# Performance work log

Measured on AMD Instinct MI355X. Metric: run time of the kernel, lower is better.

## Reference

```python
import jax, jax.numpy as jnp
import numpy as np

B, T, N, D = 64, 12, 207, 128
H, ORDER = 8, 2
HID = 2 * D  # mlp_ratio = 2


def _ln(x, g, b, eps=1e-5):
    m = x.mean(-1, keepdims=True)
    v = ((x - m) ** 2).mean(-1, keepdims=True)
    return (x - m) * jax.lax.rsqrt(v + eps) * g + b


def _l2norm(t, eps=1e-12):
    # matches torch.nn.functional.normalize(dim=-1)
    n = jnp.sqrt((t * t).sum(-1, keepdims=True))
    return t / jnp.maximum(n, eps)


def _fast_attn(q, k, v):
    # q, k, v: (B2, L, H, Dh); Performer-style linear attention from FastAttentionLayer.fast_attention
    q = _l2norm(q)
    k = _l2norm(k)
    L = q.shape[1]
    kvs = jnp.einsum('blhm,blhd->bhmd', k, v)
    num = jnp.einsum('bnhm,bhmd->bnhd', q, kvs) + L * v
    ks_sum = k.sum(axis=1)  # (B2, H, Dh)
    den = jnp.einsum('bnhm,bhm->bnh', q, ks_sum)[..., None] + L
    return num / jnp.maximum(den, 1e-5)


def _fast_layer(x, qkv_w, out_w, out_b):
    # x: (B, T, N, D). qkv_bias=False (mask arg), kernel=3 -> out_proj: Linear(2D, D)
    b, t, n, d = x.shape
    dh = d // H
    qkv = x @ qkv_w.T  # (B, T, N, 3D)
    q, k, v = jnp.split(qkv, 3, axis=-1)
    # spatial pass: attend over the N nodes for each (b, t)
    out_s = _fast_attn(q.reshape(b * t, n, H, dh),
                       k.reshape(b * t, n, H, dh),
                       v.reshape(b * t, n, H, dh)).reshape(b, t, n, d)
    # temporal pass: attend over the T steps for each (b, n)
    qt = q.transpose(0, 2, 1, 3).reshape(b * n, t, H, dh)
    kt = k.transpose(0, 2, 1, 3).reshape(b * n, t, H, dh)
    vt = v.transpose(0, 2, 1, 3).reshape(b * n, t, H, dh)
    out_t = _fast_attn(qt, kt, vt).reshape(b, n, t, d).transpose(0, 2, 1, 3)
    return jnp.concatenate([out_s, out_t], -1) @ out_w.T + out_b


def _forward(x, graph, qkv_w, out_w, out_b, pw_w, pw_b,
             fc1_w, fc1_b, fc2_w, fc2_b, ln1_g, ln1_b, ln2_g, ln2_b):
    # GraphPropagate: x_list = [x, graph @ x, ...] (Ks = ORDER hops)
    xs = [x]
    xk = x
    for _ in range(ORDER - 1):
        xk = jnp.einsum('thi,btij->bthj', graph, xk)
        xs.append(xk)
    # per-hop fast attention + zero-init pointwise branch, summed over hops
    agg = jnp.zeros_like(x)
    for i in range(ORDER):
        agg = agg + _fast_layer(xs[i], qkv_w[i], out_w[i], out_b[i]) + xs[i] @ pw_w[i].T + pw_b[i]
    h = _ln(x + agg, ln1_g, ln1_b)
    ff = jax.nn.relu(h @ fc1_w.T + fc1_b) @ fc2_w.T + fc2_b
    return _ln(h + ff, ln2_g, ln2_b)


def setup_inputs() -> dict:
    key = jax.random.key(0)
    ks = jax.random.split(key, 8)
    s = 0.02
    return {
        'x': jax.random.normal(ks[0], (B, T, N, D), jnp.float32),
        'graph': jax.random.uniform(ks[1], (T, N, N), jnp.float32) / N,
        'qkv_w': jax.random.normal(ks[2], (ORDER, 3 * D, D), jnp.float32) * s,
        'out_w': jax.random.normal(ks[3], (ORDER, D, 2 * D), jnp.float32) * s,
        'out_b': jnp.zeros((ORDER, D), jnp.float32),
        'pw_w': jax.random.normal(ks[4], (ORDER, D, D), jnp.float32) * s,
        'pw_b': jnp.zeros((ORDER, D), jnp.float32),
        'fc1_w': jax.random.normal(ks[5], (HID, D), jnp.float32) * s,
        'fc1_b': jnp.zeros((HID,), jnp.float32),
        'fc2_w': jax.random.normal(ks[6], (D, HID), jnp.float32) * s,
        'fc2_b': jnp.zeros((D,), jnp.float32),
        'ln1_g': jnp.ones((D,), jnp.float32),
        'ln1_b': jnp.zeros((D,), jnp.float32),
        'ln2_g': jnp.ones((D,), jnp.float32),
        'ln2_b': jnp.zeros((D,), jnp.float32),
    }


def reference(x, graph, qkv_w, out_w, out_b, pw_w, pw_b,
              fc1_w, fc1_b, fc2_w, fc2_b, ln1_g, ln1_b, ln2_g, ln2_b):
    return _forward(x, graph, qkv_w, out_w, out_b, pw_w, pw_b,
                    fc1_w, fc1_b, fc2_w, fc2_b, ln1_g, ln1_b, ln2_g, ln2_b)
```

## Files before the change

### kernel.cpp

```cpp
#include <hip/hip_runtime.h>
#include <hip/hip_bf16.h>

#define BB 64
#define TT 12
#define NN 207
#define DD 128
#define HH 8
#define DH 16
#define MROWS (BB*TT*NN)
#define KPAD 224
#define AW 768
#define CHB 32
#define CROWS (CHB*TT*NN)

typedef __bf16 bf16x8 __attribute__((ext_vector_type(8)));
typedef __bf16 bf16x4 __attribute__((ext_vector_type(4)));
typedef float  f32x4  __attribute__((ext_vector_type(4)));

__device__ inline float  b2f(__bf16 v){ return (float)v; }
__device__ inline __bf16 f2b(float v){ return (__bf16)v; }
__device__ inline bf16x8 ldfrag(const __bf16* p){ return *reinterpret_cast<const bf16x8*>(p); }

__device__ inline void gload_lds16(const __bf16* g, __bf16* l){
    __builtin_amdgcn_global_load_lds(
        (const __attribute__((address_space(1))) void*)(g),
        (__attribute__((address_space(3))) void*)(l), 16, 0, 0);
}
__device__ inline int swz(int r){ return (r ^ (r>>2)) & 3; }

__global__ __launch_bounds__(256) void xcopy_kernel(const float* __restrict__ x, __bf16* __restrict__ abuf)
{
    int nt = gridDim.x*256;
    for (int gIdx = blockIdx.x*256 + threadIdx.x; gIdx < MROWS*16; gIdx += nt) {
        int row = gIdx >> 4, c8 = (gIdx & 15)*8;
        const float* s = x + (size_t)row*DD + c8;
        f32x4 a = *reinterpret_cast<const f32x4*>(s);
        f32x4 b = *reinterpret_cast<const f32x4*>(s+4);
        bf16x8 r;
        #pragma unroll
        for (int i=0;i<4;i++){ r[i] = f2b(a[i]); r[i+4] = f2b(b[i]); }
        *reinterpret_cast<bf16x8*>(abuf + (size_t)row*AW + c8) = r;
    }
}

__global__ __launch_bounds__(256) void prep_misc_kernel(
    const float* __restrict__ graph, const float* __restrict__ qkv_w,
    const float* __restrict__ out_w, const float* __restrict__ out_b,
    const float* __restrict__ pw_w,  const float* __restrict__ pw_b,
    const float* __restrict__ fc1_w, const float* __restrict__ fc2_w,
    __bf16* __restrict__ gpad, __bf16* __restrict__ qkv_wb, __bf16* __restrict__ wcomb,
    __bf16* __restrict__ fc1_wb, __bf16* __restrict__ fc2_wb, float* __restrict__ bias_comb)
{
    int nt = gridDim.x*256;
    int tid = blockIdx.x*256 + threadIdx.x;
    for (int i = tid; i < TT*NN*KPAD; i += nt) {
        int k = i % KPAD, r = i / KPAD;
        gpad[i] = (k < NN) ? f2b(graph[(size_t)r*NN + k]) : f2b(0.f);
    }
    for (int i = tid; i < 2*3*DD*DD; i += nt) qkv_wb[i] = f2b(qkv_w[i]);
    for (int i = tid; i < DD*AW; i += nt) {
        int c = i / AW, j = i % AW;
        float v;
        if      (j < 128) v = pw_w[c*128 + j];
        else if (j < 256) v = pw_w[128*128 + c*128 + (j-128)];
        else if (j < 512) v = out_w[c*256 + (j-256)];
        else              v = out_w[128*256 + c*256 + (j-512)];
        wcomb[i] = f2b(v);
    }
    for (int i = tid; i < 2*DD*DD; i += nt) fc1_wb[i] = f2b(fc1_w[i]);
    for (int i = tid; i < 2*DD*DD; i += nt) fc2_wb[i] = f2b(fc2_w[i]);
    for (int i = tid; i < DD; i += nt)
        bias_comb[i] = pw_b[i] + pw_b[128+i] + out_b[i] + out_b[128+i];
}

__global__ __launch_bounds__(256) void propagate_kernel(const __bf16* __restrict__ gp,
    __bf16* __restrict__ abuf)
{
    int bt   = blockIdx.x;
    int t    = bt % TT;
    int tile = blockIdx.y;
    int lane = threadIdx.x & 63, w = threadIdx.x >> 6;
    int lhi = lane >> 4, llo = lane & 15;
    __shared__ __attribute__((aligned(16))) __bf16 XT[DD][40];
    const __bf16* xbt  = abuf + (size_t)bt*NN*AW;
    const __bf16* grow = gp + (size_t)t*NN*KPAD;
    int rowbase = tile*64 + w*16;
    f32x4 acc[8];
    #pragma unroll
    for (int i=0;i<8;i++) acc[i] = (f32x4){0.f,0.f,0.f,0.f};
    int arow = rowbase + llo; if (arow > NN-1) arow = NN-1;
    for (int k0=0; k0<KPAD; k0+=32) {
        __syncthreads();
        for (int kl = (threadIdx.x>>7); kl < 32; kl += 2) {
            int kk = k0 + kl, c = threadIdx.x & 127;
            XT[c][kl] = (kk < NN) ? xbt[(size_t)kk*AW + c] : f2b(0.f);
        }
        __syncthreads();
        bf16x8 a = ldfrag(grow + (size_t)arow*KPAD + k0 + lhi*8);
        #pragma unroll
        for (int cf=0;cf<8;cf++){
            bf16x8 b = *reinterpret_cast<const bf16x8*>(&XT[cf*16+llo][lhi*8]);
            acc[cf] = __builtin_amdgcn_mfma_f32_16x16x32_bf16(a, b, acc[cf], 0,0,0);
        }
    }
    #pragma unroll
    for (int e=0;e<4;e++){
        int row = rowbase + lhi*4 + e;
        if (row < NN) {
            #pragma unroll
            for (int cf=0;cf<8;cf++)
                abuf[((size_t)bt*NN + row)*AW + DD + cf*16 + llo] = f2b(acc[cf][e]);
        }
    }
}

template<int MODE, bool RELU>
__global__ __launch_bounds__(512) void gemm_kernel(const __bf16* __restrict__ A, size_t lda,
    const __bf16* __restrict__ W, const float* __restrict__ bias,
    void* out, size_t ldc, int K, int mend,
    const __bf16* __restrict__ resid, size_t ldr,
    const float* __restrict__ lng, const float* __restrict__ lnb)
{
    __shared__ __attribute__((aligned(16))) __bf16 lds[3][12288];
    int w = threadIdx.x >> 6, lane = threadIdx.x & 63;
    int lhi = lane >> 4, llo = lane & 15;
    size_t row0 = (size_t)blockIdx.x*256;
    int col0 = blockIdx.y*128;
    int nt = K >> 5;

    int sA0 = (w*2+0)*64 + lane, sA1 = (w*2+1)*64 + lane, sW = w*64 + lane;
    int rA0 = sA0>>2, uA0 = sA0&3, rA1 = sA1>>2, uA1 = sA1&3, rW = sW>>2, uW = sW&3;
    long gr0 = (long)row0 + rA0; if (gr0 >= mend) gr0 = mend-1;
    long gr1 = (long)row0 + rA1; if (gr1 >= mend) gr1 = mend-1;
    const __bf16* gA0 = A + (size_t)gr0*lda + ((uA0 ^ swz(rA0))<<3);
    const __bf16* gA1 = A + (size_t)gr1*lda + ((uA1 ^ swz(rA1))<<3);
    const __bf16* gW  = W + (size_t)(col0 + rW)*K + ((uW ^ swz(rW))<<3);
    __bf16* base0 = &lds[0][0];

    int aoff[2], woff[8];
    #pragma unroll
    for (int rt=0;rt<2;rt++){
        int rl = w*32 + rt*16 + llo;
        aoff[rt] = rl*32 + ((lhi ^ swz(rl))<<3);
    }
    #pragma unroll
    for (int cf=0;cf<8;cf++){
        int wr = cf*16 + llo;
        woff[cf] = 8192 + wr*32 + ((lhi ^ swz(wr))<<3);
    }

    f32x4 acc[2][8];
    #pragma unroll
    for (int i=0;i<2;i++)
        #pragma unroll
        for (int j=0;j<8;j++) acc[i][j] = (f32x4){0.f,0.f,0.f,0.f};

    #define STAGE(buf, tt) { int k0 = (tt)<<5; __bf16* Lw = base0 + (buf)*12288;           \
        gload_lds16(gA0 + k0, Lw + (w*2+0)*512);                                           \
        gload_lds16(gA1 + k0, Lw + (w*2+1)*512);                                           \
        gload_lds16(gW  + k0, Lw + 8192 + w*512); }

    STAGE(0,0); STAGE(1,1); STAGE(2,2);

    int cur = 0;
    for (int t = 0; t < nt; ++t) {
        if (t <= nt-3)      asm volatile("s_waitcnt vmcnt(6)" ::: "memory");
        else if (t == nt-2) asm volatile("s_waitcnt vmcnt(3)" ::: "memory");
        else                asm volatile("s_waitcnt vmcnt(0)" ::: "memory");
        __builtin_amdgcn_s_barrier();
        __builtin_amdgcn_sched_barrier(0);
        const __bf16* Lb = base0 + cur*12288;
        bf16x8 a[2], b[8];
        #pragma unroll
        for (int rt=0;rt<2;rt++) a[rt] = *reinterpret_cast<const bf16x8*>(&Lb[aoff[rt]]);
        #pragma unroll
        for (int cf=0;cf<8;cf++)  b[cf] = *reinterpret_cast<const bf16x8*>(&Lb[woff[cf]]);
        asm volatile("s_waitcnt lgkmcnt(0)" ::: "memory");
        __builtin_amdgcn_sched_barrier(0);
        __builtin_amdgcn_s_barrier();
        if (t+3 < nt) STAGE(cur, t+3);
        #pragma unroll
        for (int rt=0;rt<2;rt++)
            #pragma unroll
            for (int cf=0;cf<8;cf++)
                acc[rt][cf] = __builtin_amdgcn_mfma_f32_16x16x32_bf16(a[rt], b[cf], acc[rt][cf], 0,0,0);
        cur = (cur == 2) ? 0 : cur + 1;
    }
    #undef STAGE

    float bv[8];
    #pragma unroll
    for (int cf=0;cf<8;cf++) bv[cf] = bias ? bias[col0 + cf*16 + llo] : 0.f;

    if (MODE == 0) {
        #pragma unroll
        for (int rt=0;rt<2;rt++) {
            #pragma unroll
            for (int e=0;e<4;e++) {
                size_t row = row0 + (size_t)w*32 + rt*16 + lhi*4 + e;
                if ((long)row >= mend) continue;
                #pragma unroll
                for (int cf=0;cf<8;cf++) {
                    float v = acc[rt][cf][e] + bv[cf];
                    if (RELU) v = fmaxf(v, 0.f);
                    ((__bf16*)out)[row*ldc + col0 + cf*16 + llo] = f2b(v);
                }
            }
        }
    } else {
        float g8[8], b8[8];
        #pragma unroll
        for (int cf=0;cf<8;cf++){ int c = cf*16 + llo; g8[cf] = lng[c]; b8[cf] = lnb[c]; }
        #pragma unroll
        for (int rt=0;rt<2;rt++) {
            #pragma unroll
            for (int e=0;e<4;e++) {
                size_t row = row0 + (size_t)w*32 + rt*16 + lhi*4 + e;
                if ((long)row >= mend) continue;
                float vals[8], s = 0.f, ss = 0.f;
                #pragma unroll
                for (int cf=0;cf<8;cf++) {
                    int c = cf*16 + llo;
                    float r = b2f(resid[row*ldr + c]);
                    float v = acc[rt][cf][e] + bv[cf] + r;
                    vals[cf] = v; s += v; ss += v*v;
                }
                #pragma unroll
                for (int o=1;o<16;o<<=1){ s += __shfl_xor(s,o,64); ss += __shfl_xor(ss,o,64); }
                float mean = s * (1.f/DD);
                float var  = ss * (1.f/DD) - mean*mean;
                float rs   = rsqrtf(var + 1e-5f);
                #pragma unroll
                for (int cf=0;cf<8;cf++) {
                    float v = (vals[cf]-mean)*rs*g8[cf] + b8[cf];
                    size_t idx = row*ldc + cf*16 + llo;
                    if (MODE == 3) ((__bf16*)out)[idx] = f2b(v);
                    else           ((float*)out)[idx]  = v;
                }
            }
        }
    }
}

template<bool RELU>
__global__ __launch_bounds__(256) void sgemm_k128(const __bf16* __restrict__ A, size_t lda,
    const __bf16* __restrict__ W, const float* __restrict__ bias,
    __bf16* __restrict__ out, size_t ldc, int ngroups)
{
    __shared__ __attribute__((aligned(16))) __bf16 lds[12][2048];
    int w = threadIdx.x >> 6, lane = threadIdx.x & 63;
    int lhi = lane >> 4, llo = lane & 15;
    int col0 = blockIdx.y*128;

    bf16x8 wf[4][8];
    #pragma unroll
    for (int ks=0;ks<4;ks++)
        #pragma unroll
        for (int cf=0;cf<8;cf++)
            wf[ks][cf] = ldfrag(W + (size_t)(col0 + cf*16 + llo)*128 + ks*32 + lhi*8);

    f32x4 bvv[8];
    #pragma unroll
    for (int cf=0;cf<8;cf++){
        if (bias) bvv[cf] = *reinterpret_cast<const f32x4*>(bias + col0 + cf*16 + lhi*4);
        else      bvv[cf] = (f32x4){0.f,0.f,0.f,0.f};
    }

    size_t gsrc[4];
    #pragma unroll
    for (int j=0;j<4;j++){
        int r = j*4 + lhi;
        int u = llo ^ r;
        gsrc[j] = (size_t)r*lda + (size_t)u*8;
    }
    int aoff[4];
    #pragma unroll
    for (int ks=0;ks<4;ks++) aoff[ks] = llo*128 + (((ks<<2)|lhi) ^ llo)*8;

    int gw = blockIdx.x*4 + w, stride = gridDim.x*4;
    int n = (gw < ngroups) ? ((ngroups-1-gw)/stride + 1) : 0;
    __bf16* slab0 = &lds[w*3][0];

    #define SSTAGE(i) { size_t rbase = (size_t)(gw + (size_t)(i)*stride)*16*lda;           \
        __bf16* L = slab0 + ((i)%3)*2048;                                                  \
        gload_lds16(A + rbase + gsrc[0], L);                                               \
        gload_lds16(A + rbase + gsrc[1], L + 512);                                         \
        gload_lds16(A + rbase + gsrc[2], L + 1024);                                        \
        gload_lds16(A + rbase + gsrc[3], L + 1536); }

    if (n > 0) SSTAGE(0);
    if (n > 1) SSTAGE(1);

    for (int i = 0; i < n; ++i) {
        int kept = ((i+1 < n) ? 4 : 0) + ((i >= 2) ? 16 : i*8);
        if      (kept >= 20) asm volatile("s_waitcnt vmcnt(20)" ::: "memory");
        else if (kept == 16) asm volatile("s_waitcnt vmcnt(16)" ::: "memory");
        else if (kept == 12) asm volatile("s_waitcnt vmcnt(12)" ::: "memory");
        else if (kept == 8)  asm volatile("s_waitcnt vmcnt(8)"  ::: "memory");
        else if (kept == 4)  asm volatile("s_waitcnt vmcnt(4)"  ::: "memory");
        else                 asm volatile("s_waitcnt vmcnt(0)"  ::: "memory");

        const __bf16* Ls = slab0 + (i%3)*2048;
        bf16x8 a[4];
        #pragma unroll
        for (int ks=0;ks<4;ks++) a[ks] = *reinterpret_cast<const bf16x8*>(&Ls[aoff[ks]]);

        if (i+2 < n) SSTAGE(i+2);

        f32x4 acc[8];
        #pragma unroll
        for (int cf=0;cf<8;cf++) acc[cf] = (f32x4){0.f,0.f,0.f,0.f};
        #pragma unroll
        for (int ks=0;ks<4;ks++)
            #pragma unroll
            for (int cf=0;cf<8;cf++)
                acc[cf] = __builtin_amdgcn_mfma_f32_16x16x32_bf16(wf[ks][cf], a[ks], acc[cf], 0,0,0);

        size_t grow = (size_t)(gw + (size_t)i*stride)*16 + llo;
        #pragma unroll
        for (int cf=0;cf<8;cf++){
            bf16x4 o;
            #pragma unroll
            for (int e=0;e<4;e++){
                float v = acc[cf][e] + bvv[cf][e];
                if (RELU) v = fmaxf(v, 0.f);
                o[e] = f2b(v);
            }
            *reinterpret_cast<bf16x4*>(out + grow*ldc + col0 + cf*16 + lhi*4) = o;
        }
    }
    #undef SSTAGE
}

#define ACH 32
__global__ __launch_bounds__(256) void attn_s_kernel(const __bf16* __restrict__ qkv,
                                                     __bf16* __restrict__ outp)
{
    int bt = blockIdx.x, g = blockIdx.y;
    const __bf16* base = qkv + (size_t)bt*NN*384 + g*32;
    __shared__ __attribute__((aligned(16))) __bf16 qbuf[224][40];
    __shared__ __attribute__((aligned(16))) __bf16 vbuf[224][40];
    __shared__ __attribute__((aligned(16))) __bf16 kbuf[ACH][40];
    __shared__ float flk[4][16][17];
    __shared__ float fls[4][16];
    int tid = threadIdx.x;
    int wave = tid >> 6, lane = tid & 63;
    int h2 = tid >> 7;
    int dd = tid & 15;
    int oct = ((tid >> 4) & 3) | ((wave & 1) << 2);
    float kvs_col[16]; float ks = 0.f;
    #pragma unroll
    for (int m=0;m<16;m++) kvs_col[m] = 0.f;

    for (int c0 = 0; c0 < NN; c0 += ACH) {
        __syncthreads();
        for (int i = tid; i < ACH*12; i += 256) {
            int r = i/12, u = i%12, seg = u>>2, uu = u&3;
            int nn = c0 + r;
            bf16x8 v8 = (bf16x8){};
            if (nn < NN) v8 = *reinterpret_cast<const bf16x8*>(base + (size_t)nn*384 + seg*128 + uu*8);
            if      (seg == 0) *reinterpret_cast<bf16x8*>(&qbuf[nn][uu*8]) = v8;
            else if (seg == 1) *reinterpret_cast<bf16x8*>(&kbuf[r][uu*8])  = v8;
            else               *reinterpret_cast<bf16x8*>(&vbuf[nn][uu*8]) = v8;
        }
        __syncthreads();
        #pragma unroll
        for (int j=0;j<4;j++){
            int r = oct + 8*j; int nn = c0 + r;
            if (nn >= NN) continue;
            bf16x8 k0 = *reinterpret_cast<const bf16x8*>(&kbuf[r][h2*16]);
            bf16x8 k1 = *reinterpret_cast<const bf16x8*>(&kbuf[r][h2*16+8]);
            float sk = 0.f;
            #pragma unroll
            for (int m=0;m<8;m++){
                float a0=b2f(k0[m]), a1=b2f(k1[m]); sk += a0*a0 + a1*a1;
            }
            float iv = 1.f/fmaxf(sqrtf(sk), 1e-12f);
            float vv  = b2f(vbuf[nn][h2*16+dd]);
            float kdd = b2f(kbuf[r][h2*16+dd]);
            float t2 = iv*vv;
            #pragma unroll
            for (int m=0;m<8;m++){
                kvs_col[m]   += b2f(k0[m])*t2;
                kvs_col[m+8] += b2f(k1[m])*t2;
            }
            ks += kdd*iv;
        }
    }
    #pragma unroll
    for (int m=0;m<16;m++){
        kvs_col[m] += __shfl_xor(kvs_col[m], 16, 64);
        kvs_col[m] += __shfl_xor(kvs_col[m], 32, 64);
    }
    ks += __shfl_xor(ks, 16, 64);
    ks += __shfl_xor(ks, 32, 64);
    if (lane < 16){
        #pragma unroll
        for (int m=0;m<16;m++) flk[wave][m][lane] = kvs_col[m];
        fls[wave][lane] = ks;
    }
    __syncthreads();
    float ksr[16];
    #pragma unroll
    for (int m=0;m<16;m++){
        kvs_col[m] += flk[wave^1][m][dd];
        ksr[m] = fls[h2*2][m] + fls[h2*2+1][m];
    }

    for (int nn = oct; nn < NN; nn += 8) {
        bf16x8 q0 = *reinterpret_cast<const bf16x8*>(&qbuf[nn][h2*16]);
        bf16x8 q1 = *reinterpret_cast<const bf16x8*>(&qbuf[nn][h2*16+8]);
        float sq = 0.f, num = 0.f, den = 0.f;
        #pragma unroll
        for (int m=0;m<8;m++){
            float qm0 = b2f(q0[m]), qm1 = b2f(q1[m]);
            sq  += qm0*qm0 + qm1*qm1;
            num += qm0*kvs_col[m] + qm1*kvs_col[m+8];
            den += qm0*ksr[m]     + qm1*ksr[m+8];
        }
        float iq = 1.f/fmaxf(sqrtf(sq), 1e-12f);
        float vv = b2f(vbuf[nn][h2*16+dd]);
        float o = (num*iq + (float)NN*vv) / fmaxf(den*iq + (float)NN, 1e-5f);
        outp[((size_t)bt*NN + nn)*AW + g*32 + h2*16 + dd] = f2b(o);
    }
}

__global__ __launch_bounds__(256) void attn_t_kernel(const __bf16* __restrict__ qkv,
                                                     __bf16* __restrict__ outp)
{
    int b = blockIdx.x;
    int nn0 = blockIdx.y * 2;
    __shared__ __attribute__((aligned(16))) __bf16 rows[TT][2][384];
    __shared__ float invq[2][TT][8], invk2[2][TT][8];
    int tid = threadIdx.x;
    for (int i = tid; i < TT*2*48; i += 256) {
        int t = i / 96, rem = i % 96;
        int nl = rem / 48, g = rem % 48;
        int nn = nn0 + nl;
        bf16x8 v8 = (bf16x8){};
        if (nn < NN) v8 = *reinterpret_cast<const bf16x8*>(qkv + ((size_t)(b*TT+t)*NN + nn)*384 + g*8);
        *reinterpret_cast<bf16x8*>(&rows[t][nl][g*8]) = v8;
    }
    __syncthreads();
    if (tid < 192) {
        int hh = tid & 7, t = (tid >> 3) % TT, nl = tid / 96;
        bf16x8 q0 = *reinterpret_cast<const bf16x8*>(&rows[t][nl][hh*16]);
        bf16x8 q1 = *reinterpret_cast<const bf16x8*>(&rows[t][nl][hh*16+8]);
        bf16x8 k0 = *reinterpret_cast<const bf16x8*>(&rows[t][nl][128+hh*16]);
        bf16x8 k1 = *reinterpret_cast<const bf16x8*>(&rows[t][nl][128+hh*16+8]);
        float sq = 0.f, sk = 0.f;
        #pragma unroll
        for (int m=0;m<8;m++){
            float a0=b2f(q0[m]), a1=b2f(q1[m]); sq += a0*a0 + a1*a1;
            float c0v=b2f(k0[m]), c1=b2f(k1[m]); sk += c0v*c0v + c1*c1;
        }
        invq[nl][t][hh]  = 1.f/fmaxf(sqrtf(sq), 1e-12f);
        invk2[nl][t][hh] = 1.f/fmaxf(sqrtf(sk), 1e-12f);
    }
    __syncthreads();
    int dd = tid & 15, h = (tid >> 4) & 7, nl = tid >> 7;
    int nn = nn0 + nl;
    float kvs_col[16], ksum[16];
    #pragma unroll
    for (int m=0;m<16;m++){ kvs_col[m]=0.f; ksum[m]=0.f; }
    #pragma unroll
    for (int t=0;t<TT;t++){
        float iv = invk2[nl][t][h];
        bf16x8 k0 = *reinterpret_cast<const bf16x8*>(&rows[t][nl][128+h*16]);
        bf16x8 k1 = *reinterpret_cast<const bf16x8*>(&rows[t][nl][128+h*16+8]);
        float vv = b2f(rows[t][nl][256+h*16+dd]);
        float t2 = iv*vv;
        #pragma unroll
        for (int m=0;m<8;m++){
            float km0 = b2f(k0[m]), km1 = b2f(k1[m]);
            kvs_col[m]   += km0*t2;  ksum[m]   += km0*iv;
            kvs_col[m+8] += km1*t2;  ksum[m+8] += km1*iv;
        }
    }
    #pragma unroll
    for (int t=0;t<TT;t++){
        float iq = invq[nl][t][h];
        bf16x8 q0 = *reinterpret_cast<const bf16x8*>(&rows[t][nl][h*16]);
        bf16x8 q1 = *reinterpret_cast<const bf16x8*>(&rows[t][nl][h*16+8]);
        float num = 0.f, den = 0.f;
        #pragma unroll
        for (int m=0;m<8;m++){
            float qm0 = b2f(q0[m]), qm1 = b2f(q1[m]);
            num += qm0*kvs_col[m]  + qm1*kvs_col[m+8];
            den += qm0*ksum[m]     + qm1*ksum[m+8];
        }
        float vv = b2f(rows[t][nl][256+h*16+dd]);
        float o = (num*iq + (float)TT*vv) / fmaxf(den*iq + (float)TT, 1e-5f);
        if (nn < NN)
            outp[((size_t)(b*TT+t)*NN + nn)*AW + h*16 + dd] = f2b(o);
    }
}

extern "C" void kernel_launch(void* const* d_in, const int* in_sizes, int n_in,
                              void* d_out, int out_size, void* d_ws, size_t ws_size,
                              hipStream_t stream)
{
    const float* x     = (const float*)d_in[0];
    const float* graph = (const float*)d_in[1];
    const float* qkv_w = (const float*)d_in[2];
    const float* out_w = (const float*)d_in[3];
    const float* out_b = (const float*)d_in[4];
    const float* pw_w  = (const float*)d_in[5];
    const float* pw_b  = (const float*)d_in[6];
    const float* fc1_w = (const float*)d_in[7];
    const float* fc1_b = (const float*)d_in[8];
    const float* fc2_w = (const float*)d_in[9];
    const float* fc2_b = (const float*)d_in[10];
    const float* ln1g  = (const float*)d_in[11];
    const float* ln1b  = (const float*)d_in[12];
    const float* ln2g  = (const float*)d_in[13];
    const float* ln2b  = (const float*)d_in[14];
    (void)in_sizes; (void)n_in; (void)out_size; (void)ws_size;

    char* ws = (char*)d_ws;
    size_t off = 0;
    __bf16* abuf = (__bf16*)(ws + off); off += (size_t)MROWS*AW*2;
    __bf16* qkvc = (__bf16*)(ws + off); off += (size_t)CROWS*3*DD*2;
    __bf16* gpad = (__bf16*)(ws + off); off += (size_t)TT*NN*KPAD*2;
    __bf16* qkv_wb = (__bf16*)(ws + off); off += (size_t)2*3*DD*DD*2;
    __bf16* wcomb  = (__bf16*)(ws + off); off += (size_t)DD*AW*2;
    __bf16* fc1_wb = (__bf16*)(ws + off); off += (size_t)2*DD*DD*2;
    __bf16* fc2_wb = (__bf16*)(ws + off); off += (size_t)2*DD*DD*2;
    float*  bias_comb = (float*)(ws + off); off += DD*4;

    dim3 blk(256), blk512(512);

    xcopy_kernel<<<dim3(4096), blk, 0, stream>>>(x, abuf);
    prep_misc_kernel<<<dim3(1024), blk, 0, stream>>>(graph, qkv_w, out_w, out_b, pw_w, pw_b,
        fc1_w, fc2_w, gpad, qkv_wb, wcomb, fc1_wb, fc2_wb, bias_comb);
    propagate_kernel<<<dim3(BB*TT, 4), blk, 0, stream>>>(gpad, abuf);

    for (int hop = 0; hop < 2; ++hop) {
        for (int c = 0; c < BB/CHB; ++c) {
            size_t rowoff = (size_t)c*CROWS;
            sgemm_k128<false><<<dim3(170, 3), blk, 0, stream>>>(
                abuf + rowoff*AW + hop*DD, (size_t)AW, qkv_wb + (size_t)hop*3*DD*DD, nullptr,
                qkvc, (size_t)(3*DD), CROWS/16);
            attn_s_kernel<<<dim3(CHB*TT, 4), blk, 0, stream>>>(
                qkvc, abuf + rowoff*AW + 256 + hop*256);
            attn_t_kernel<<<dim3(CHB, (NN+1)/2), blk, 0, stream>>>(
                qkvc, abuf + rowoff*AW + 384 + hop*256);
        }
    }

    gemm_kernel<3,false><<<dim3(MROWS/256, 1), blk512, 0, stream>>>(
        abuf, (size_t)AW, wcomb, bias_comb, (void*)abuf, (size_t)AW, AW, MROWS,
        abuf, (size_t)AW, ln1g, ln1b);
    sgemm_k128<true><<<dim3(256, 2), blk, 0, stream>>>(
        abuf, (size_t)AW, fc1_wb, fc1_b, abuf + 256, (size_t)AW, MROWS/16);
    gemm_kernel<4,false><<<dim3(MROWS/256, 1), blk512, 0, stream>>>(
        abuf + 256, (size_t)AW, fc2_wb, fc2_b, d_out, (size_t)DD, 2*DD, MROWS,
        abuf, (size_t)AW, ln2g, ln2b);
}
```

Before: 840.8 us.

## Fuse FFN into one kernel, merge attention launches, fold x cast into propagate

Adds an ffn_kernel that computes fc1+ReLU, fc2, the residual and LayerNorm per 128-row tile. The hidden activation stays in LDS instead of going through global memory, and two launches are dropped. The separate spatial and temporal attention kernels are merged into one launch with a block-index split. The standalone fp32-to-bf16 copy of x is removed: propagate now reads fp32 x and writes the bf16 copy itself. Weights in the fused FFN are read directly from global/cache per wave, which may add load pressure.

```diff
diff --git a/kernel.cpp b/kernel.cpp
--- a/kernel.cpp
+++ b/kernel.cpp
@@ -27,21 +27,6 @@
         (__attribute__((address_space(3))) void*)(l), 16, 0, 0);
 }
 __device__ inline int swz(int r){ return (r ^ (r>>2)) & 3; }
-
-__global__ __launch_bounds__(256) void xcopy_kernel(const float* __restrict__ x, __bf16* __restrict__ abuf)
-{
-    int nt = gridDim.x*256;
-    for (int gIdx = blockIdx.x*256 + threadIdx.x; gIdx < MROWS*16; gIdx += nt) {
-        int row = gIdx >> 4, c8 = (gIdx & 15)*8;
-        const float* s = x + (size_t)row*DD + c8;
-        f32x4 a = *reinterpret_cast<const f32x4*>(s);
-        f32x4 b = *reinterpret_cast<const f32x4*>(s+4);
-        bf16x8 r;
-        #pragma unroll
-        for (int i=0;i<4;i++){ r[i] = f2b(a[i]); r[i+4] = f2b(b[i]); }
-        *reinterpret_cast<bf16x8*>(abuf + (size_t)row*AW + c8) = r;
-    }
-}
 
 __global__ __launch_bounds__(256) void prep_misc_kernel(
     const float* __restrict__ graph, const float* __restrict__ qkv_w,
@@ -74,7 +59,7 @@
 }
 
 __global__ __launch_bounds__(256) void propagate_kernel(const __bf16* __restrict__ gp,
-    __bf16* __restrict__ abuf)
+    const float* __restrict__ x, __bf16* __restrict__ abuf)
 {
     int bt   = blockIdx.x;
     int t    = bt % TT;
@@ -82,7 +67,7 @@
     int lane = threadIdx.x & 63, w = threadIdx.x >> 6;
     int lhi = lane >> 4, llo = lane & 15;
     __shared__ __attribute__((aligned(16))) __bf16 XT[DD][40];
-    const __bf16* xbt  = abuf + (size_t)bt*NN*AW;
+    const float*  xbt  = x  + (size_t)bt*NN*DD;
     const __bf16* grow = gp + (size_t)t*NN*KPAD;
     int rowbase = tile*64 + w*16;
     f32x4 acc[8];
@@ -93,7 +78,10 @@
         __syncthreads();
         for (int kl = (threadIdx.x>>7); kl < 32; kl += 2) {
             int kk = k0 + kl, c = threadIdx.x & 127;
-            XT[c][kl] = (kk < NN) ? xbt[(size_t)kk*AW + c] : f2b(0.f);
+            __bf16 xb = (kk < NN) ? f2b(xbt[(size_t)kk*DD + c]) : f2b(0.f);
+            XT[c][kl] = xb;
+            if (kk < NN && (kk>>6) == tile)
+                abuf[((size_t)bt*NN + kk)*AW + c] = xb;
         }
         __syncthreads();
         bf16x8 a = ldfrag(grow + (size_t)arow*KPAD + k0 + lhi*8);
@@ -233,9 +221,7 @@
                 #pragma unroll
                 for (int cf=0;cf<8;cf++) {
                     float v = (vals[cf]-mean)*rs*g8[cf] + b8[cf];
-                    size_t idx = row*ldc + cf*16 + llo;
-                    if (MODE == 3) ((__bf16*)out)[idx] = f2b(v);
-                    else           ((float*)out)[idx]  = v;
+                    ((__bf16*)out)[row*ldc + cf*16 + llo] = f2b(v);
                 }
             }
         }
@@ -332,167 +318,320 @@
     #undef SSTAGE
 }
 
+__global__ __launch_bounds__(256) void ffn_kernel(const __bf16* __restrict__ h,
+    const __bf16* __restrict__ w1, const float* __restrict__ b1,
+    const __bf16* __restrict__ w2, const float* __restrict__ b2,
+    const float* __restrict__ lng, const float* __restrict__ lnb,
+    float* __restrict__ dout)
+{
+    __shared__ __attribute__((aligned(16))) __bf16 hring[3][4096];
+    __shared__ __attribute__((aligned(16))) __bf16 f1b[8192];
+    __shared__ float fl2[32][4][2];
+    int w = threadIdx.x >> 6, lane = threadIdx.x & 63;
+    int lhi = lane >> 4, llo = lane & 15;
+    size_t row0 = (size_t)blockIdx.x * 128;
+
+    size_t gsrc[2]; int ldst[2];
+    #pragma unroll
+    for (int j=0;j<2;j++){
+        int i = w*64 + lane + 256*j;
+        int r = i >> 4, u = i & 15;
+        gsrc[j] = (size_t)r*AW + ((u ^ (r & 15)) << 3);
+        ldst[j] = (w*64 + 256*j) * 8;
+    }
+    #define FSTAGE(slot, g) { const __bf16* src = h + (row0 + (size_t)(g)*32)*AW;          \
+        gload_lds16(src + gsrc[0], &hring[slot][0] + ldst[0]);                             \
+        gload_lds16(src + gsrc[1], &hring[slot][0] + ldst[1]); }
+
+    f32x4 b1v[4], b2v[2], gv[2], bt2[2];
+    #pragma unroll
+    for (int c4=0;c4<4;c4++) b1v[c4] = *reinterpret_cast<const f32x4*>(b1 + w*64 + c4*16 + lhi*4);
+    #pragma unroll
+    for (int c2=0;c2<2;c2++){
+        b2v[c2] = *reinterpret_cast<const f32x4*>(b2  + w*32 + c2*16 + lhi*4);
+        gv[c2]  = *reinterpret_cast<const f32x4*>(lng + w*32 + c2*16 + lhi*4);
+        bt2[c2] = *reinterpret_cast<const f32x4*>(lnb + w*32 + c2*16 + lhi*4);
+    }
+
+    FSTAGE(0,0); FSTAGE(1,1); FSTAGE(2,2);
+
+    for (int g = 0; g < 4; ++g) {
+        if (g < 2)       asm volatile("s_waitcnt vmcnt(4)" ::: "memory");
+        else if (g == 2) asm volatile("s_waitcnt vmcnt(2)" ::: "memory");
+        else             asm volatile("s_waitcnt vmcnt(0)" ::: "memory");
+        __builtin_amdgcn_s_barrier();
+        __builtin_amdgcn_sched_barrier(0);
+        const __bf16* Hs = &hring[g % 3][0];
+
+        bf16x8 hb[2][4];
+        bf16x4 hres[2][2];
+        #pragma unroll
+        for (int rf=0;rf<2;rf++){
+            int r = rf*16 + llo;
+            #pragma unroll
+            for (int ks=0;ks<4;ks++)
+                hb[rf][ks] = *reinterpret_cast<const bf16x8*>(Hs + r*128 + (((ks*4+lhi) ^ llo) << 3));
+            #pragma unroll
+            for (int cf=0;cf<2;cf++){
+                int unit = w*4 + cf*2 + (lhi>>1);
+                hres[cf][rf] = *reinterpret_cast<const bf16x4*>(Hs + r*128 + ((unit ^ llo) << 3) + (lhi & 1)*4);
+            }
+        }
+        asm volatile("s_waitcnt lgkmcnt(0)" ::: "memory");
+        __builtin_amdgcn_sched_barrier(0);
+        __builtin_amdgcn_s_barrier();
+        if (g + 3 < 4) FSTAGE(g % 3, g + 3);
+
+        f32x4 acc1[4][2];
+        #pragma unroll
+        for (int i=0;i<4;i++){ acc1[i][0] = (f32x4){0,0,0,0}; acc1[i][1] = (f32x4){0,0,0,0}; }
+        #pragma unroll
+        for (int ks=0;ks<4;ks++){
+            #pragma unroll
+            for (int cf2=0;cf2<4;cf2++){
+                bf16x8 wfr = ldfrag(w1 + (size_t)(w*64 + cf2*16 + llo)*128 + ks*32 + lhi*8);
+                #pragma unroll
+                for (int rf=0;rf<2;rf++)
+                    acc1[cf2][rf] = __builtin_amdgcn_mfma_f32_16x16x32_bf16(wfr, hb[rf][ks], acc1[cf2][rf], 0,0,0);
+            }
+        }
+        #pragma unroll
+        for (int rf=0;rf<2;rf++){
+            int r = rf*16 + llo;
+            #pragma unroll
+            for (int cf2=0;cf2<4;cf2++){
+                bf16x4 o;
+                #pragma unroll
+                for (int e=0;e<4;e++) o[e] = f2b(fmaxf(acc1[cf2][rf][e] + b1v[cf2][e], 0.f));
+                int unit = w*8 + cf2*2 + (lhi>>1);
+                *reinterpret_cast<bf16x4*>(&f1b[r*256 + ((unit ^ r) << 3) + (lhi&1)*4]) = o;
+            }
+        }
+        asm volatile("s_waitcnt lgkmcnt(0)" ::: "memory");
+        __builtin_amdgcn_sched_barrier(0);
+        __builtin_amdgcn_s_barrier();
+
+        f32x4 acc2[2][2];
+        acc2[0][0]=(f32x4){0,0,0,0}; acc2[0][1]=(f32x4){0,0,0,0};
+        acc2[1][0]=(f32x4){0,0,0,0}; acc2[1][1]=(f32x4){0,0,0,0};
+        #pragma unroll
+        for (int ks2=0;ks2<8;ks2++){
+            bf16x8 fb[2];
+            #pragma unroll
+            for (int rf=0;rf<2;rf++){
+                int r = rf*16 + llo;
+                fb[rf] = *reinterpret_cast<const bf16x8*>(&f1b[r*256 + (((ks2*4+lhi) ^ r) << 3)]);
+            }
+            #pragma unroll
+            for (int cf=0;cf<2;cf++){
+                bf16x8 wfr = ldfrag(w2 + (size_t)(w*32 + cf*16 + llo)*256 + ks2*32 + lhi*8);
+                #pragma unroll
+                for (int rf=0;rf<2;rf++)
+                    acc2[cf][rf] = __builtin_amdgcn_mfma_f32_16x16x32_bf16(wfr, fb[rf], acc2[cf][rf], 0,0,0);
+            }
+        }
+
+        float vals[2][2][4]; float s[2] = {0.f,0.f}, ss[2] = {0.f,0.f};
+        #pragma unroll
+        for (int rf=0;rf<2;rf++)
+            #pragma unroll
+            for (int cf=0;cf<2;cf++)
+                #pragma unroll
+                for (int e=0;e<4;e++){
+                    float v = acc2[cf][rf][e] + b2v[cf][e] + b2f(hres[cf][rf][e]);
+                    vals[rf][cf][e] = v; s[rf] += v; ss[rf] += v*v;
+                }
+        #pragma unroll
+        for (int rf=0;rf<2;rf++){
+            s[rf]  += __shfl_xor(s[rf],16,64);  s[rf]  += __shfl_xor(s[rf],32,64);
+            ss[rf] += __shfl_xor(ss[rf],16,64); ss[rf] += __shfl_xor(ss[rf],32,64);
+            if (lhi == 0){ fl2[rf*16+llo][w][0] = s[rf]; fl2[rf*16+llo][w][1] = ss[rf]; }
+        }
+        asm volatile("s_waitcnt lgkmcnt(0)" ::: "memory");
+        __builtin_amdgcn_s_barrier();
+        #pragma unroll
+        for (int rf=0;rf<2;rf++){
+            int r = rf*16 + llo;
+            float S  = fl2[r][0][0]+fl2[r][1][0]+fl2[r][2][0]+fl2[r][3][0];
+            float SS = fl2[r][0][1]+fl2[r][1][1]+fl2[r][2][1]+fl2[r][3][1];
+            float mean = S*(1.f/DD), var = SS*(1.f/DD)-mean*mean, rs = rsqrtf(var+1e-5f);
+            size_t grow = row0 + (size_t)g*32 + r;
+            #pragma unroll
+            for (int cf=0;cf<2;cf++){
+                f32x4 o;
+                #pragma unroll
+                for (int e=0;e<4;e++) o[e] = (vals[rf][cf][e]-mean)*rs*gv[cf][e] + bt2[cf][e];
+                *reinterpret_cast<f32x4*>(dout + grow*DD + w*32 + cf*16 + lhi*4) = o;
+            }
+        }
+        __builtin_amdgcn_s_barrier();
+    }
+    #undef FSTAGE
+}
+
 #define ACH 32
-__global__ __launch_bounds__(256) void attn_s_kernel(const __bf16* __restrict__ qkv,
-                                                     __bf16* __restrict__ outp)
+#define SBLKS (CHB*TT*4)
+__global__ __launch_bounds__(256) void attn_st_kernel(const __bf16* __restrict__ qkv,
+    __bf16* __restrict__ outs, __bf16* __restrict__ outt)
 {
-    int bt = blockIdx.x, g = blockIdx.y;
-    const __bf16* base = qkv + (size_t)bt*NN*384 + g*32;
-    __shared__ __attribute__((aligned(16))) __bf16 qbuf[224][40];
-    __shared__ __attribute__((aligned(16))) __bf16 vbuf[224][40];
-    __shared__ __attribute__((aligned(16))) __bf16 kbuf[ACH][40];
-    __shared__ float flk[4][16][17];
-    __shared__ float fls[4][16];
+    __shared__ __attribute__((aligned(16))) char smem[44032];
     int tid = threadIdx.x;
-    int wave = tid >> 6, lane = tid & 63;
-    int h2 = tid >> 7;
-    int dd = tid & 15;
-    int oct = ((tid >> 4) & 3) | ((wave & 1) << 2);
-    float kvs_col[16]; float ks = 0.f;
-    #pragma unroll
-    for (int m=0;m<16;m++) kvs_col[m] = 0.f;
-
-    for (int c0 = 0; c0 < NN; c0 += ACH) {
+    int bx = blockIdx.x;
+
+    if (bx < SBLKS) {
+        int bt = bx >> 2, g = bx & 3;
+        const __bf16* base = qkv + (size_t)bt*NN*384 + g*32;
+        __bf16 (*qbuf)[40] = (__bf16(*)[40])(smem);
+        __bf16 (*vbuf)[40] = (__bf16(*)[40])(smem + 17920);
+        __bf16 (*kbuf)[40] = (__bf16(*)[40])(smem + 35840);
+        float (*flk)[16][17] = (float(*)[16][17])(smem + 38400);
+        float (*fls)[16]     = (float(*)[16])(smem + 42752);
+        int wave = tid >> 6, lane = tid & 63;
+        int h2 = tid >> 7;
+        int dd = tid & 15;
+        int oct = ((tid >> 4) & 3) | ((wave & 1) << 2);
+        float kvs_col[16]; float ks = 0.f;
+        #pragma unroll
+        for (int m=0;m<16;m++) kvs_col[m] = 0.f;
+
+        for (int c0 = 0; c0 < NN; c0 += ACH) {
+            __syncthreads();
+            for (int i = tid; i < ACH*12; i += 256) {
+                int r = i/12, u = i%12, seg = u>>2, uu = u&3;
+                int nn = c0 + r;
+                bf16x8 v8 = (bf16x8){};
+                if (nn < NN) v8 = *reinterpret_cast<const bf16x8*>(base + (size_t)nn*384 + seg*128 + uu*8);
+                if      (seg == 0) *reinterpret_cast<bf16x8*>(&qbuf[nn][uu*8]) = v8;
+                else if (seg == 1) *reinterpret_cast<bf16x8*>(&kbuf[r][uu*8])  = v8;
+                else               *reinterpret_cast<bf16x8*>(&vbuf[nn][uu*8]) = v8;
+            }
+            __syncthreads();
+            #pragma unroll
+            for (int j=0;j<4;j++){
+                int r = oct + 8*j; int nn = c0 + r;
+                if (nn >= NN) continue;
+                bf16x8 k0 = *reinterpret_cast<const bf16x8*>(&kbuf[r][h2*16]);
+                bf16x8 k1 = *reinterpret_cast<const bf16x8*>(&kbuf[r][h2*16+8]);
+                float sk = 0.f;
+                #pragma unroll
+                for (int m=0;m<8;m++){
+                    float a0=b2f(k0[m]), a1=b2f(k1[m]); sk += a0*a0 + a1*a1;
+                }
+                float iv = 1.f/fmaxf(sqrtf(sk), 1e-12f);
+                float vv  = b2f(vbuf[nn][h2*16+dd]);
+                float kdd = b2f(kbuf[r][h2*16+dd]);
+                float t2 = iv*vv;
+                #pragma unroll
+                for (int m=0;m<8;m++){
+                    kvs_col[m]   += b2f(k0[m])*t2;
+                    kvs_col[m+8] += b2f(k1[m])*t2;
+                }
+                ks += kdd*iv;
+            }
+        }
+        #pragma unroll
+        for (int m=0;m<16;m++){
+            kvs_col[m] += __shfl_xor(kvs_col[m], 16, 64);
+            kvs_col[m] += __shfl_xor(kvs_col[m], 32, 64);
+        }
+        ks += __shfl_xor(ks, 16, 64);
+        ks += __shfl_xor(ks, 32, 64);
+        if (lane < 16){
+            #pragma unroll
+            for (int m=0;m<16;m++) flk[wave][m][lane] = kvs_col[m];
+            fls[wave][lane] = ks;
+        }
         __syncthreads();
-        for (int i = tid; i < ACH*12; i += 256) {
-            int r = i/12, u = i%12, seg = u>>2, uu = u&3;
-            int nn = c0 + r;
+        float ksr[16];
+        #pragma unroll
+        for (int m=0;m<16;m++){
+            kvs_col[m] += flk[wave^1][m][dd];
+            ksr[m] = fls[h2*2][m] + fls[h2*2+1][m];
+        }
+        for (int nn = oct; nn < NN; nn += 8) {
+            bf16x8 q0 = *reinterpret_cast<const bf16x8*>(&qbuf[nn][h2*16]);
+            bf16x8 q1 = *reinterpret_cast<const bf16x8*>(&qbuf[nn][h2*16+8]);
+            float sq = 0.f, num = 0.f, den = 0.f;
+            #pragma unroll
+            for (int m=0;m<8;m++){
+                float qm0 = b2f(q0[m]), qm1 = b2f(q1[m]);
+                sq  += qm0*qm0 + qm1*qm1;
+                num += qm0*kvs_col[m] + qm1*kvs_col[m+8];
+                den += qm0*ksr[m]     + qm1*ksr[m+8];
+            }
+            float iq = 1.f/fmaxf(sqrtf(sq), 1e-12f);
+            float vv = b2f(vbuf[nn][h2*16+dd]);
+            float o = (num*iq + (float)NN*vv) / fmaxf(den*iq + (float)NN, 1e-5f);
+            outs[((size_t)bt*NN + nn)*AW + g*32 + h2*16 + dd] = f2b(o);
+        }
+    } else {
+        int tix = bx - SBLKS;
+        int b = tix / 104;
+        int nn0 = (tix % 104) * 2;
+        __bf16 (*rows)[2][384] = (__bf16(*)[2][384])(smem);
+        float (*invq)[TT][8]  = (float(*)[TT][8])(smem + 18432);
+        float (*invk2)[TT][8] = (float(*)[TT][8])(smem + 19200);
+        for (int i = tid; i < TT*2*48; i += 256) {
+            int t = i / 96, rem = i % 96;
+            int nl = rem / 48, g = rem % 48;
+            int nn = nn0 + nl;
             bf16x8 v8 = (bf16x8){};
-            if (nn < NN) v8 = *reinterpret_cast<const bf16x8*>(base + (size_t)nn*384 + seg*128 + uu*8);
-            if      (seg == 0) *reinterpret_cast<bf16x8*>(&qbuf[nn][uu*8]) = v8;
-            else if (seg == 1) *reinterpret_cast<bf16x8*>(&kbuf[r][uu*8])  = v8;
-            else               *reinterpret_cast<bf16x8*>(&vbuf[nn][uu*8]) = v8;
+            if (nn < NN) v8 = *reinterpret_cast<const bf16x8*>(qkv + ((size_t)(b*TT+t)*NN + nn)*384 + g*8);
+            *reinterpret_cast<bf16x8*>(&rows[t][nl][g*8]) = v8;
         }
         __syncthreads();
-        #pragma unroll
-        for (int j=0;j<4;j++){
-            int r = oct + 8*j; int nn = c0 + r;
-            if (nn >= NN) continue;
-            bf16x8 k0 = *reinterpret_cast<const bf16x8*>(&kbuf[r][h2*16]);
-            bf16x8 k1 = *reinterpret_cast<const bf16x8*>(&kbuf[r][h2*16+8]);
-            float sk = 0.f;
+        if (tid < 192) {
+            int hh = tid & 7, t = (tid >> 3) % TT, nl = tid / 96;
+            bf16x8 q0 = *reinterpret_cast<const bf16x8*>(&rows[t][nl][hh*16]);
+            bf16x8 q1 = *reinterpret_cast<const bf16x8*>(&rows[t][nl][hh*16+8]);
+            bf16x8 k0 = *reinterpret_cast<const bf16x8*>(&rows[t][nl][128+hh*16]);
+            bf16x8 k1 = *reinterpret_cast<const bf16x8*>(&rows[t][nl][128+hh*16+8]);
+            float sq = 0.f, sk = 0.f;
             #pragma unroll
             for (int m=0;m<8;m++){
-                float a0=b2f(k0[m]), a1=b2f(k1[m]); sk += a0*a0 + a1*a1;
-            }
-            float iv = 1.f/fmaxf(sqrtf(sk), 1e-12f);
-            float vv  = b2f(vbuf[nn][h2*16+dd]);
-            float kdd = b2f(kbuf[r][h2*16+dd]);
+                float a0=b2f(q0[m]), a1=b2f(q1[m]); sq += a0*a0 + a1*a1;
+                float c0v=b2f(k0[m]), c1=b2f(k1[m]); sk += c0v*c0v + c1*c1;
+            }
+            invq[nl][t][hh]  = 1.f/fmaxf(sqrtf(sq), 1e-12f);
+            invk2[nl][t][hh] = 1.f/fmaxf(sqrtf(sk), 1e-12f);
+        }
+        __syncthreads();
+        int dd = tid & 15, h = (tid >> 4) & 7, nl = tid >> 7;
+        int nn = nn0 + nl;
+        float kvs_col[16], ksum[16];
+        #pragma unroll
+        for (int m=0;m<16;m++){ kvs_col[m]=0.f; ksum[m]=0.f; }
+        #pragma unroll
+        for (int t=0;t<TT;t++){
+            float iv = invk2[nl][t][h];
+            bf16x8 k0 = *reinterpret_cast<const bf16x8*>(&rows[t][nl][128+h*16]);
+            bf16x8 k1 = *reinterpret_cast<const bf16x8*>(&rows[t][nl][128+h*16+8]);
+            float vv = b2f(rows[t][nl][256+h*16+dd]);
             float t2 = iv*vv;
             #pragma unroll
             for (int m=0;m<8;m++){
-                kvs_col[m]   += b2f(k0[m])*t2;
-                kvs_col[m+8] += b2f(k1[m])*t2;
-            }
-            ks += kdd*iv;
-        }
-    }
-    #pragma unroll
-    for (int m=0;m<16;m++){
-        kvs_col[m] += __shfl_xor(kvs_col[m], 16, 64);
-        kvs_col[m] += __shfl_xor(kvs_col[m], 32, 64);
-    }
-    ks += __shfl_xor(ks, 16, 64);
-    ks += __shfl_xor(ks, 32, 64);
-    if (lane < 16){
-        #pragma unroll
-        for (int m=0;m<16;m++) flk[wave][m][lane] = kvs_col[m];
-        fls[wave][lane] = ks;
-    }
-    __syncthreads();
-    float ksr[16];
-    #pragma unroll
-    for (int m=0;m<16;m++){
-        kvs_col[m] += flk[wave^1][m][dd];
-        ksr[m] = fls[h2*2][m] + fls[h2*2+1][m];
-    }
-
-    for (int nn = oct; nn < NN; nn += 8) {
-        bf16x8 q0 = *reinterpret_cast<const bf16x8*>(&qbuf[nn][h2*16]);
-        bf16x8 q1 = *reinterpret_cast<const bf16x8*>(&qbuf[nn][h2*16+8]);
-        float sq = 0.f, num = 0.f, den = 0.f;
-        #pragma unroll
-        for (int m=0;m<8;m++){
-            float qm0 = b2f(q0[m]), qm1 = b2f(q1[m]);
-            sq  += qm0*qm0 + qm1*qm1;
-            num += qm0*kvs_col[m] + qm1*kvs_col[m+8];
-            den += qm0*ksr[m]     + qm1*ksr[m+8];
-        }
-        float iq = 1.f/fmaxf(sqrtf(sq), 1e-12f);
-        float vv = b2f(vbuf[nn][h2*16+dd]);
-        float o = (num*iq + (float)NN*vv) / fmaxf(den*iq + (float)NN, 1e-5f);
-        outp[((size_t)bt*NN + nn)*AW + g*32 + h2*16 + dd] = f2b(o);
-    }
-}
-
-__global__ __launch_bounds__(256) void attn_t_kernel(const __bf16* __restrict__ qkv,
-                                                     __bf16* __restrict__ outp)
-{
-    int b = blockIdx.x;
-    int nn0 = blockIdx.y * 2;
-    __shared__ __attribute__((aligned(16))) __bf16 rows[TT][2][384];
-    __shared__ float invq[2][TT][8], invk2[2][TT][8];
-    int tid = threadIdx.x;
-    for (int i = tid; i < TT*2*48; i += 256) {
-        int t = i / 96, rem = i % 96;
-        int nl = rem / 48, g = rem % 48;
-        int nn = nn0 + nl;
-        bf16x8 v8 = (bf16x8){};
-        if (nn < NN) v8 = *reinterpret_cast<const bf16x8*>(qkv + ((size_t)(b*TT+t)*NN + nn)*384 + g*8);
-        *reinterpret_cast<bf16x8*>(&rows[t][nl][g*8]) = v8;
-    }
-    __syncthreads();
-    if (tid < 192) {
-        int hh = tid & 7, t = (tid >> 3) % TT, nl = tid / 96;
-        bf16x8 q0 = *reinterpret_cast<const bf16x8*>(&rows[t][nl][hh*16]);
-        bf16x8 q1 = *reinterpret_cast<const bf16x8*>(&rows[t][nl][hh*16+8]);
-        bf16x8 k0 = *reinterpret_cast<const bf16x8*>(&rows[t][nl][128+hh*16]);
-        bf16x8 k1 = *reinterpret_cast<const bf16x8*>(&rows[t][nl][128+hh*16+8]);
-        float sq = 0.f, sk = 0.f;
-        #pragma unroll
-        for (int m=0;m<8;m++){
-            float a0=b2f(q0[m]), a1=b2f(q1[m]); sq += a0*a0 + a1*a1;
-            float c0v=b2f(k0[m]), c1=b2f(k1[m]); sk += c0v*c0v + c1*c1;
-        }
-        invq[nl][t][hh]  = 1.f/fmaxf(sqrtf(sq), 1e-12f);
-        invk2[nl][t][hh] = 1.f/fmaxf(sqrtf(sk), 1e-12f);
-    }
-    __syncthreads();
-    int dd = tid & 15, h = (tid >> 4) & 7, nl = tid >> 7;
-    int nn = nn0 + nl;
-    float kvs_col[16], ksum[16];
-    #pragma unroll
-    for (int m=0;m<16;m++){ kvs_col[m]=0.f; ksum[m]=0.f; }
-    #pragma unroll
-    for (int t=0;t<TT;t++){
-        float iv = invk2[nl][t][h];
-        bf16x8 k0 = *reinterpret_cast<const bf16x8*>(&rows[t][nl][128+h*16]);
-        bf16x8 k1 = *reinterpret_cast<const bf16x8*>(&rows[t][nl][128+h*16+8]);
-        float vv = b2f(rows[t][nl][256+h*16+dd]);
-        float t2 = iv*vv;
-        #pragma unroll
-        for (int m=0;m<8;m++){
-            float km0 = b2f(k0[m]), km1 = b2f(k1[m]);
-            kvs_col[m]   += km0*t2;  ksum[m]   += km0*iv;
-            kvs_col[m+8] += km1*t2;  ksum[m+8] += km1*iv;
-        }
-    }
-    #pragma unroll
-    for (int t=0;t<TT;t++){
-        float iq = invq[nl][t][h];
-        bf16x8 q0 = *reinterpret_cast<const bf16x8*>(&rows[t][nl][h*16]);
-        bf16x8 q1 = *reinterpret_cast<const bf16x8*>(&rows[t][nl][h*16+8]);
-        float num = 0.f, den = 0.f;
-        #pragma unroll
-        for (int m=0;m<8;m++){
-            float qm0 = b2f(q0[m]), qm1 = b2f(q1[m]);
-            num += qm0*kvs_col[m]  + qm1*kvs_col[m+8];
-            den += qm0*ksum[m]     + qm1*ksum[m+8];
-        }
-        float vv = b2f(rows[t][nl][256+h*16+dd]);
-        float o = (num*iq + (float)TT*vv) / fmaxf(den*iq + (float)TT, 1e-5f);
-        if (nn < NN)
-            outp[((size_t)(b*TT+t)*NN + nn)*AW + h*16 + dd] = f2b(o);
+                float km0 = b2f(k0[m]), km1 = b2f(k1[m]);
+                kvs_col[m]   += km0*t2;  ksum[m]   += km0*iv;
+                kvs_col[m+8] += km1*t2;  ksum[m+8] += km1*iv;
+            }
+        }
+        #pragma unroll
+        for (int t=0;t<TT;t++){
+            float iq = invq[nl][t][h];
+            bf16x8 q0 = *reinterpret_cast<const bf16x8*>(&rows[t][nl][h*16]);
+            bf16x8 q1 = *reinterpret_cast<const bf16x8*>(&rows[t][nl][h*16+8]);
+            float num = 0.f, den = 0.f;
+            #pragma unroll
+            for (int m=0;m<8;m++){
+                float qm0 = b2f(q0[m]), qm1 = b2f(q1[m]);
+                num += qm0*kvs_col[m]  + qm1*kvs_col[m+8];
+                den += qm0*ksum[m]     + qm1*ksum[m+8];
+            }
+            float vv = b2f(rows[t][nl][256+h*16+dd]);
+            float o = (num*iq + (float)TT*vv) / fmaxf(den*iq + (float)TT, 1e-5f);
+            if (nn < NN)
+                outt[((size_t)(b*TT+t)*NN + nn)*AW + h*16 + dd] = f2b(o);
+        }
     }
 }
 
@@ -530,10 +669,9 @@
 
     dim3 blk(256), blk512(512);
 
-    xcopy_kernel<<<dim3(4096), blk, 0, stream>>>(x, abuf);
     prep_misc_kernel<<<dim3(1024), blk, 0, stream>>>(graph, qkv_w, out_w, out_b, pw_w, pw_b,
         fc1_w, fc2_w, gpad, qkv_wb, wcomb, fc1_wb, fc2_wb, bias_comb);
-    propagate_kernel<<<dim3(BB*TT, 4), blk, 0, stream>>>(gpad, abuf);
+    propagate_kernel<<<dim3(BB*TT, 4), blk, 0, stream>>>(gpad, x, abuf);
 
     for (int hop = 0; hop < 2; ++hop) {
         for (int c = 0; c < BB/CHB; ++c) {
@@ -541,19 +679,14 @@
             sgemm_k128<false><<<dim3(170, 3), blk, 0, stream>>>(
                 abuf + rowoff*AW + hop*DD, (size_t)AW, qkv_wb + (size_t)hop*3*DD*DD, nullptr,
                 qkvc, (size_t)(3*DD), CROWS/16);
-            attn_s_kernel<<<dim3(CHB*TT, 4), blk, 0, stream>>>(
-                qkvc, abuf + rowoff*AW + 256 + hop*256);
-            attn_t_kernel<<<dim3(CHB, (NN+1)/2), blk, 0, stream>>>(
-                qkvc, abuf + rowoff*AW + 384 + hop*256);
+            attn_st_kernel<<<dim3(SBLKS + CHB*104), blk, 0, stream>>>(
+                qkvc, abuf + rowoff*AW + 256 + hop*256, abuf + rowoff*AW + 384 + hop*256);
         }
     }
 
     gemm_kernel<3,false><<<dim3(MROWS/256, 1), blk512, 0, stream>>>(
         abuf, (size_t)AW, wcomb, bias_comb, (void*)abuf, (size_t)AW, AW, MROWS,
         abuf, (size_t)AW, ln1g, ln1b);
-    sgemm_k128<true><<<dim3(256, 2), blk, 0, stream>>>(
-        abuf, (size_t)AW, fc1_wb, fc1_b, abuf + 256, (size_t)AW, MROWS/16);
-    gemm_kernel<4,false><<<dim3(MROWS/256, 1), blk512, 0, stream>>>(
-        abuf + 256, (size_t)AW, fc2_wb, fc2_b, d_out, (size_t)DD, 2*DD, MROWS,
-        abuf, (size_t)AW, ln2g, ln2b);
-}
+    ffn_kernel<<<dim3(MROWS/128), blk, 0, stream>>>(
+        abuf, fc1_wb, fc1_b, fc2_wb, fc2_b, ln2g, ln2b, (float*)d_out);
+}
```

Result: slower. 870.4 us (+3.5%).
